# Performance work log

Measured on AMD Instinct MI355X. Metric: run time of the kernel, lower is better.

The kernel has to match this reference:

```python
import jax, jax.numpy as jnp
import numpy as np

N, IN_DIM, OUT_DIM, HEADS = 8192, 256, 128, 2


def setup_inputs() -> dict:
    key = jax.random.key(0)
    k1, k2, k3, k4, k5 = jax.random.split(key, 5)
    features = jax.random.normal(k1, (N, IN_DIM), dtype=jnp.float32)
    adjacency = jax.random.randint(k2, (N, N), 0, 2, dtype=jnp.int32)
    # nn.Linear(input_dim, output_dim*heads, bias=False): weight [out, in]
    W = jax.random.normal(k3, (OUT_DIM * HEADS, IN_DIM), dtype=jnp.float32) * 0.05
    attn_src = jax.random.normal(k4, (HEADS, OUT_DIM), dtype=jnp.float32) * 0.05
    attn_dst = jax.random.normal(k5, (HEADS, OUT_DIM), dtype=jnp.float32) * 0.05
    return {"features": features, "adjacency": adjacency, "W": W,
            "attn_src": attn_src, "attn_dst": attn_dst}


def reference(features, adjacency, W, attn_src, attn_dst):
    n = features.shape[0]
    # transformed: [N, H, F]
    transformed = (features @ W.T).reshape(n, HEADS, OUT_DIM)
    src_scores = jnp.einsum('nhf,hf->nh', transformed, attn_src)  # [N, H]
    dst_scores = jnp.einsum('nhf,hf->nh', transformed, attn_dst)  # [N, H]
    # logits: [N_src, N_dst, H]
    logits = jax.nn.leaky_relu(src_scores[:, None, :] + dst_scores[None, :, :],
                               negative_slope=0.2)
    mask = adjacency > 0  # [N, N]
    logits = jnp.where(mask[:, :, None], logits, -jnp.inf)
    attention = jax.nn.softmax(logits, axis=1)  # softmax over dst dim (dim=1)
    attention = jnp.nan_to_num(attention, nan=0.0, posinf=0.0, neginf=0.0)
    aggregated = jnp.einsum('ijh,jhf->ihf', attention, transformed)  # [N, H, F]
    return aggregated.mean(axis=1)  # [N, F]
```

## Files before the change

kernel.cpp:

```cpp
#include <hip/hip_runtime.h>
#include <stdint.h>
#include <stddef.h>

#define NN 8192
#define KD 256
#define CD 256
#define FD 128
#define BI 32
#define BJ 64
#define JSPLIT 2
#define JCHUNK (NN / JSPLIT)

typedef __attribute__((ext_vector_type(4))) float f32x4;
typedef __attribute__((ext_vector_type(8))) short b16x8;

__device__ __forceinline__ unsigned short f2bf(float x) {
    unsigned int u = __float_as_uint(x);
    u += 0x7fffu + ((u >> 16) & 1u);
    return (unsigned short)(u >> 16);
}

__global__ __launch_bounds__(256) void k_transform(
    const float* __restrict__ feat, const float* __restrict__ W,
    float* __restrict__ T)
{
    __shared__ unsigned short a_lds[64 * 32];
    __shared__ unsigned short b_lds[256 * 32];
    const int t = threadIdx.x;
    const int wave = t >> 6, lane = t & 63;
    const int l15 = lane & 15, quad = lane >> 4;
    const int n0 = blockIdx.x * 64;
    const int ai = t >> 2, ag = t & 3;

    f32x4 acc[4][4] = {};
    for (int kc = 0; kc < 8; ++kc) {
        const int k0 = kc * 32;
        __syncthreads();
        {
            const float* src = feat + (size_t)(n0 + ai) * KD + k0 + ag * 8;
            const float4 v0 = *(const float4*)src;
            const float4 v1 = *(const float4*)(src + 4);
            union { unsigned short us[8]; b16x8 v; } pk;
            pk.us[0] = f2bf(v0.x); pk.us[1] = f2bf(v0.y);
            pk.us[2] = f2bf(v0.z); pk.us[3] = f2bf(v0.w);
            pk.us[4] = f2bf(v1.x); pk.us[5] = f2bf(v1.y);
            pk.us[6] = f2bf(v1.z); pk.us[7] = f2bf(v1.w);
            const int slot = ag ^ ((ai >> 1) & 3);
            *(b16x8*)&a_lds[ai * 32 + slot * 8] = pk.v;
        }
        for (int p = 0; p < 4; ++p) {
            const int G = p * 256 + t;
            const int c = G >> 2, g = G & 3;
            const float* src = W + (size_t)c * KD + k0 + g * 8;
            const float4 v0 = *(const float4*)src;
            const float4 v1 = *(const float4*)(src + 4);
            union { unsigned short us[8]; b16x8 v; } pk;
            pk.us[0] = f2bf(v0.x); pk.us[1] = f2bf(v0.y);
            pk.us[2] = f2bf(v0.z); pk.us[3] = f2bf(v0.w);
            pk.us[4] = f2bf(v1.x); pk.us[5] = f2bf(v1.y);
            pk.us[6] = f2bf(v1.z); pk.us[7] = f2bf(v1.w);
            const int slot = g ^ ((c >> 1) & 3);
            *(b16x8*)&b_lds[c * 32 + slot * 8] = pk.v;
        }
        __syncthreads();
        b16x8 af[4], bfr[4];
        for (int mt = 0; mt < 4; ++mt) {
            const int m = mt * 16 + l15;
            af[mt] = *(const b16x8*)&a_lds[m * 32 + (quad ^ ((m >> 1) & 3)) * 8];
        }
        for (int nt = 0; nt < 4; ++nt) {
            const int c = wave * 64 + nt * 16 + l15;
            bfr[nt] = *(const b16x8*)&b_lds[c * 32 + (quad ^ ((c >> 1) & 3)) * 8];
        }
        for (int mt = 0; mt < 4; ++mt)
            for (int nt = 0; nt < 4; ++nt)
                acc[mt][nt] = __builtin_amdgcn_mfma_f32_16x16x32_bf16(
                    af[mt], bfr[nt], acc[mt][nt], 0, 0, 0);
    }
    for (int mt = 0; mt < 4; ++mt)
        for (int nt = 0; nt < 4; ++nt)
            for (int r = 0; r < 4; ++r) {
                const int n = n0 + mt * 16 + quad * 4 + r;
                const int c = wave * 64 + nt * 16 + l15;
                T[(size_t)n * CD + c] = acc[mt][nt][r];
            }
}

__global__ __launch_bounds__(256) void k_scores(
    const float* __restrict__ T, const float* __restrict__ asrc,
    const float* __restrict__ adst, float* __restrict__ s, float* __restrict__ dsc)
{
    const int wave = threadIdx.x >> 6, lane = threadIdx.x & 63;
    const int n = blockIdx.x * 4 + wave;
    const float* tr = T + (size_t)n * CD;
    const float t0 = tr[lane], t1 = tr[lane + 64], t2 = tr[lane + 128], t3 = tr[lane + 192];
    float s0 = t0 * asrc[lane] + t1 * asrc[lane + 64];
    float s1 = t2 * asrc[128 + lane] + t3 * asrc[192 + lane];
    float d0 = t0 * adst[lane] + t1 * adst[lane + 64];
    float d1 = t2 * adst[128 + lane] + t3 * adst[192 + lane];
    for (int m = 1; m < 64; m <<= 1) {
        s0 += __shfl_xor(s0, m); s1 += __shfl_xor(s1, m);
        d0 += __shfl_xor(d0, m); d1 += __shfl_xor(d1, m);
    }
    if (lane == 0) {
        s[n * 2 + 0] = s0; s[n * 2 + 1] = s1;
        dsc[n * 2 + 0] = d0; dsc[n * 2 + 1] = d1;
    }
}

__global__ __launch_bounds__(256) void k_transpose(
    const float* __restrict__ T, unsigned short* __restrict__ Tt)
{
    __shared__ float tile[64][65];
    const int t = threadIdx.x;
    const int n0 = blockIdx.x * 64, c0 = blockIdx.y * 64;
    for (int p = 0; p < 4; ++p) {
        const int idx = p * 256 + t;
        const int r = idx >> 4, q = idx & 15;
        const float4 v = *(const float4*)(T + (size_t)(n0 + r) * CD + c0 + q * 4);
        tile[r][q * 4 + 0] = v.x; tile[r][q * 4 + 1] = v.y;
        tile[r][q * 4 + 2] = v.z; tile[r][q * 4 + 3] = v.w;
    }
    __syncthreads();
    for (int p = 0; p < 16; ++p) {
        const int idx = p * 256 + t;
        const int c = idx >> 6, n = idx & 63;
        Tt[(size_t)(c0 + c) * NN + n0 + n] = f2bf(tile[n][c]);
    }
}

__global__ __launch_bounds__(256) void k_gat(
    const int* __restrict__ adj, const unsigned short* __restrict__ Tt,
    const float* __restrict__ s, const float* __restrict__ d,
    float* __restrict__ num_part,
    float* __restrict__ den_part)
{
    __shared__ unsigned short tt_lds[CD * BJ];
    __shared__ unsigned short w_lds[2 * BI * BJ];
    __shared__ float d_lds[2][BJ];

    const int t = threadIdx.x;
    const int wave = t >> 6, lane = t & 63;
    const int l15 = lane & 15, quad = lane >> 4;
    const int i0 = blockIdx.x * BI;
    const int chunk = blockIdx.y;
    const int jbase = chunk * JCHUNK;

    const int wi = t >> 3;
    const int j8 = t & 7;
    const int gi = i0 + wi;
    const float s0 = s[gi * 2 + 0];
    const float s1 = s[gi * 2 + 1];

    const int h = wave >> 1;
    const int fh = wave & 1;
    const int cbase = h * 128 + fh * 64;

    f32x4 acc[2][4] = {};
    float den0 = 0.f, den1 = 0.f;

    for (int jt = 0; jt < JCHUNK / BJ; ++jt) {
        const int j0 = jbase + jt * BJ;
        __syncthreads();
        for (int p = 0; p < 8; ++p) {
            const int G = p * 256 + t;
            const int c = G >> 3, g = G & 7;
            const b16x8 v = *(const b16x8*)(Tt + (size_t)c * NN + j0 + g * 8);
            *(b16x8*)&tt_lds[c * BJ + ((g ^ (c & 7)) << 3)] = v;
        }
        if (t < 128) d_lds[t & 1][t >> 1] = d[(j0 + (t >> 1)) * 2 + (t & 1)];
        const int* arow = adj + (size_t)gi * NN + j0 + j8 * 8;
        const int4 a0 = *(const int4*)arow;
        const int4 a1 = *(const int4*)(arow + 4);
        __syncthreads();
        const int am[8] = {a0.x, a0.y, a0.z, a0.w, a1.x, a1.y, a1.z, a1.w};
        union { unsigned short us[8]; b16x8 v; } w0, w1;
        float dp0 = 0.f, dp1 = 0.f;
        for (int e = 0; e < 8; ++e) {
            const float dd0 = d_lds[0][j8 * 8 + e];
            const float dd1 = d_lds[1][j8 * 8 + e];
            float x0 = s0 + dd0;  x0 = x0 > 0.f ? x0 : 0.2f * x0;
            float x1 = s1 + dd1;  x1 = x1 > 0.f ? x1 : 0.2f * x1;
            const float e0 = am[e] != 0 ? __expf(x0) : 0.f;
            const float e1 = am[e] != 0 ? __expf(x1) : 0.f;
            dp0 += e0; dp1 += e1;
            w0.us[e] = f2bf(e0); w1.us[e] = f2bf(e1);
        }
        den0 += dp0; den1 += dp1;
        const int slot = (j8 ^ (wi & 7)) << 3;
        *(b16x8*)&w_lds[(0 * BI + wi) * BJ + slot] = w0.v;
        *(b16x8*)&w_lds[(1 * BI + wi) * BJ + slot] = w1.v;
        __syncthreads();
        for (int ks = 0; ks < 2; ++ks) {
            const int gidx = ks * 4 + quad;
            b16x8 af[2], bfr[4];
            for (int mt = 0; mt < 2; ++mt) {
                const int m = mt * 16 + l15;
                af[mt] = *(const b16x8*)&w_lds[(h * BI + m) * BJ + ((gidx ^ (m & 7)) << 3)];
            }
            for (int nt = 0; nt < 4; ++nt) {
                const int c = cbase + nt * 16 + l15;
                bfr[nt] = *(const b16x8*)&tt_lds[c * BJ + ((gidx ^ (c & 7)) << 3)];
            }
            for (int mt = 0; mt < 2; ++mt)
                for (int nt = 0; nt < 4; ++nt)
                    acc[mt][nt] = __builtin_amdgcn_mfma_f32_16x16x32_bf16(
                        af[mt], bfr[nt], acc[mt][nt], 0, 0, 0);
        }
    }
    den0 += __shfl_xor(den0, 1); den0 += __shfl_xor(den0, 2); den0 += __shfl_xor(den0, 4);
    den1 += __shfl_xor(den1, 1); den1 += __shfl_xor(den1, 2); den1 += __shfl_xor(den1, 4);
    if (j8 == 0) {
        den_part[((size_t)chunk * 2 + 0) * NN + gi] = den0;
        den_part[((size_t)chunk * 2 + 1) * NN + gi] = den1;
    }
    float* np_ = num_part + (size_t)chunk * NN * CD;
    for (int mt = 0; mt < 2; ++mt)
        for (int nt = 0; nt < 4; ++nt)
            for (int r = 0; r < 4; ++r) {
                const int n = i0 + mt * 16 + quad * 4 + r;
                const int c = cbase + nt * 16 + l15;
                np_[(size_t)n * CD + c] = acc[mt][nt][r];
            }
}

__global__ __launch_bounds__(256) void k_combine(
    const float* __restrict__ num_part, const float* __restrict__ den_part,
    float* __restrict__ out)
{
    const int idx = blockIdx.x * 256 + threadIdx.x;
    const int n = idx >> 7, f = idx & 127;
    const size_t row = (size_t)n * CD;
    const float n0 = num_part[row + f] + num_part[(size_t)NN * CD + row + f];
    const float n1 = num_part[row + 128 + f] + num_part[(size_t)NN * CD + row + 128 + f];
    const float d0 = den_part[n] + den_part[2 * NN + n];
    const float d1 = den_part[NN + n] + den_part[3 * NN + n];
    const float r0 = d0 != 0.f ? n0 / d0 : 0.f;
    const float r1 = d1 != 0.f ? n1 / d1 : 0.f;
    out[idx] = 0.5f * (r0 + r1);
}

extern "C" void kernel_launch(void* const* d_in, const int* in_sizes, int n_in,
                              void* d_out, int out_size, void* d_ws, size_t ws_size,
                              hipStream_t stream) {
    const float* feat = (const float*)d_in[0];
    const int*   adj  = (const int*)d_in[1];
    const float* W    = (const float*)d_in[2];
    const float* asrc = (const float*)d_in[3];
    const float* adst = (const float*)d_in[4];
    float* out = (float*)d_out;

    char* ws = (char*)d_ws;
    unsigned short* Tt = (unsigned short*)ws;
    float* T   = (float*)(ws + ((size_t)4 << 20));
    float* s   = (float*)(ws + ((size_t)12 << 20));
    float* dsc = (float*)(ws + ((size_t)12 << 20) + 65536);
    float* den = (float*)(ws + ((size_t)12 << 20) + 131072);
    float* nump= (float*)(ws + ((size_t)12 << 20) + 262144);

    k_transform<<<128, 256, 0, stream>>>(feat, W, T);
    k_scores<<<2048, 256, 0, stream>>>(T, asrc, adst, s, dsc);
    k_transpose<<<dim3(128, 4), 256, 0, stream>>>(T, Tt);
    k_gat<<<dim3(NN / BI, JSPLIT), 256, 0, stream>>>(adj, Tt, s, dsc, nump, den);
    k_combine<<<NN * FD / 256, 256, 0, stream>>>(nump, den, out);
}
```

Measured before the change: 501.8 us.

## Fuse scores and transpose into transform; async LDS loads and wider j-split in GAT

New measurement: 462.6 us. -7.8%, faster.

```diff
diff --git a/kernel.cpp b/kernel.cpp
--- a/kernel.cpp
+++ b/kernel.cpp
@@ -8,8 +8,6 @@
 #define FD 128
 #define BI 32
 #define BJ 64
-#define JSPLIT 2
-#define JCHUNK (NN / JSPLIT)
 
 typedef __attribute__((ext_vector_type(4))) float f32x4;
 typedef __attribute__((ext_vector_type(8))) short b16x8;
@@ -20,12 +18,23 @@
     return (unsigned short)(u >> 16);
 }
 
+__device__ __forceinline__ void async16(const void* g, void* l) {
+    __builtin_amdgcn_global_load_lds(
+        (const __attribute__((address_space(1))) unsigned int*)g,
+        (__attribute__((address_space(3))) unsigned int*)l, 16, 0, 0);
+}
+
 __global__ __launch_bounds__(256) void k_transform(
     const float* __restrict__ feat, const float* __restrict__ W,
-    float* __restrict__ T)
+    const float* __restrict__ asrc, const float* __restrict__ adst,
+    unsigned short* __restrict__ Tt, float* __restrict__ s, float* __restrict__ d)
 {
     __shared__ unsigned short a_lds[64 * 32];
     __shared__ unsigned short b_lds[256 * 32];
+    __shared__ unsigned short tr_lds[256 * 72];
+    __shared__ float sc_lds[4][64];
+    __shared__ float dc_lds[4][64];
+
     const int t = threadIdx.x;
     const int wave = t >> 6, lane = t & 63;
     const int l15 = lane & 15, quad = lane >> 4;
@@ -77,80 +86,70 @@
                 acc[mt][nt] = __builtin_amdgcn_mfma_f32_16x16x32_bf16(
                     af[mt], bfr[nt], acc[mt][nt], 0, 0, 0);
     }
+
+    float aS[4], aD[4];
+    for (int nt = 0; nt < 4; ++nt) {
+        const int c = wave * 64 + nt * 16 + l15;
+        aS[nt] = asrc[c]; aD[nt] = adst[c];
+    }
+    for (int mt = 0; mt < 4; ++mt)
+        for (int r = 0; r < 4; ++r) {
+            float vs = 0.f, vd = 0.f;
+            for (int nt = 0; nt < 4; ++nt) {
+                const float x = acc[mt][nt][r];
+                vs += x * aS[nt]; vd += x * aD[nt];
+            }
+            vs += __shfl_xor(vs, 1); vd += __shfl_xor(vd, 1);
+            vs += __shfl_xor(vs, 2); vd += __shfl_xor(vd, 2);
+            vs += __shfl_xor(vs, 4); vd += __shfl_xor(vd, 4);
+            vs += __shfl_xor(vs, 8); vd += __shfl_xor(vd, 8);
+            if (l15 == 0) {
+                const int nl = mt * 16 + quad * 4 + r;
+                sc_lds[wave][nl] = vs; dc_lds[wave][nl] = vd;
+            }
+        }
     for (int mt = 0; mt < 4; ++mt)
         for (int nt = 0; nt < 4; ++nt)
             for (int r = 0; r < 4; ++r) {
-                const int n = n0 + mt * 16 + quad * 4 + r;
                 const int c = wave * 64 + nt * 16 + l15;
-                T[(size_t)n * CD + c] = acc[mt][nt][r];
-            }
-}
-
-__global__ __launch_bounds__(256) void k_scores(
-    const float* __restrict__ T, const float* __restrict__ asrc,
-    const float* __restrict__ adst, float* __restrict__ s, float* __restrict__ dsc)
-{
-    const int wave = threadIdx.x >> 6, lane = threadIdx.x & 63;
-    const int n = blockIdx.x * 4 + wave;
-    const float* tr = T + (size_t)n * CD;
-    const float t0 = tr[lane], t1 = tr[lane + 64], t2 = tr[lane + 128], t3 = tr[lane + 192];
-    float s0 = t0 * asrc[lane] + t1 * asrc[lane + 64];
-    float s1 = t2 * asrc[128 + lane] + t3 * asrc[192 + lane];
-    float d0 = t0 * adst[lane] + t1 * adst[lane + 64];
-    float d1 = t2 * adst[128 + lane] + t3 * adst[192 + lane];
-    for (int m = 1; m < 64; m <<= 1) {
-        s0 += __shfl_xor(s0, m); s1 += __shfl_xor(s1, m);
-        d0 += __shfl_xor(d0, m); d1 += __shfl_xor(d1, m);
-    }
-    if (lane == 0) {
-        s[n * 2 + 0] = s0; s[n * 2 + 1] = s1;
-        dsc[n * 2 + 0] = d0; dsc[n * 2 + 1] = d1;
-    }
-}
-
-__global__ __launch_bounds__(256) void k_transpose(
-    const float* __restrict__ T, unsigned short* __restrict__ Tt)
-{
-    __shared__ float tile[64][65];
-    const int t = threadIdx.x;
-    const int n0 = blockIdx.x * 64, c0 = blockIdx.y * 64;
-    for (int p = 0; p < 4; ++p) {
+                const int n = mt * 16 + quad * 4 + r;
+                tr_lds[c * 72 + n] = f2bf(acc[mt][nt][r]);
+            }
+    __syncthreads();
+    if (t < 128) {
+        const int n = t >> 1, h = t & 1;
+        s[(size_t)(n0 + n) * 2 + h] = sc_lds[h * 2][n] + sc_lds[h * 2 + 1][n];
+        d[(size_t)(n0 + n) * 2 + h] = dc_lds[h * 2][n] + dc_lds[h * 2 + 1][n];
+    }
+    for (int p = 0; p < 8; ++p) {
         const int idx = p * 256 + t;
-        const int r = idx >> 4, q = idx & 15;
-        const float4 v = *(const float4*)(T + (size_t)(n0 + r) * CD + c0 + q * 4);
-        tile[r][q * 4 + 0] = v.x; tile[r][q * 4 + 1] = v.y;
-        tile[r][q * 4 + 2] = v.z; tile[r][q * 4 + 3] = v.w;
-    }
-    __syncthreads();
-    for (int p = 0; p < 16; ++p) {
-        const int idx = p * 256 + t;
-        const int c = idx >> 6, n = idx & 63;
-        Tt[(size_t)(c0 + c) * NN + n0 + n] = f2bf(tile[n][c]);
-    }
-}
-
-__global__ __launch_bounds__(256) void k_gat(
+        const int c = idx >> 3, g = idx & 7;
+        *(b16x8*)(Tt + (size_t)c * NN + n0 + g * 8) = *(const b16x8*)&tr_lds[c * 72 + g * 8];
+    }
+}
+
+__global__ __launch_bounds__(256, 4) void k_gat(
     const int* __restrict__ adj, const unsigned short* __restrict__ Tt,
     const float* __restrict__ s, const float* __restrict__ d,
     float* __restrict__ num_part,
-    float* __restrict__ den_part)
+    float* __restrict__ den_part,
+    int jchunk)
 {
     __shared__ unsigned short tt_lds[CD * BJ];
     __shared__ unsigned short w_lds[2 * BI * BJ];
-    __shared__ float d_lds[2][BJ];
 
     const int t = threadIdx.x;
     const int wave = t >> 6, lane = t & 63;
     const int l15 = lane & 15, quad = lane >> 4;
     const int i0 = blockIdx.x * BI;
     const int chunk = blockIdx.y;
-    const int jbase = chunk * JCHUNK;
+    const int jbase = chunk * jchunk;
 
     const int wi = t >> 3;
     const int j8 = t & 7;
     const int gi = i0 + wi;
-    const float s0 = s[gi * 2 + 0];
-    const float s1 = s[gi * 2 + 1];
+    const float s0 = s[(size_t)gi * 2 + 0];
+    const float s1 = s[(size_t)gi * 2 + 1];
 
     const int h = wave >> 1;
     const int fh = wave & 1;
@@ -158,29 +157,30 @@
 
     f32x4 acc[2][4] = {};
     float den0 = 0.f, den1 = 0.f;
-
-    for (int jt = 0; jt < JCHUNK / BJ; ++jt) {
+    const int njt = jchunk / BJ;
+
+    for (int jt = 0; jt < njt; ++jt) {
         const int j0 = jbase + jt * BJ;
         __syncthreads();
-        for (int p = 0; p < 8; ++p) {
-            const int G = p * 256 + t;
-            const int c = G >> 3, g = G & 7;
-            const b16x8 v = *(const b16x8*)(Tt + (size_t)c * NN + j0 + g * 8);
-            *(b16x8*)&tt_lds[c * BJ + ((g ^ (c & 7)) << 3)] = v;
-        }
-        if (t < 128) d_lds[t & 1][t >> 1] = d[(j0 + (t >> 1)) * 2 + (t & 1)];
         const int* arow = adj + (size_t)gi * NN + j0 + j8 * 8;
         const int4 a0 = *(const int4*)arow;
         const int4 a1 = *(const int4*)(arow + 4);
-        __syncthreads();
+        const float4* dvp = (const float4*)(d + (size_t)(j0 + j8 * 8) * 2);
+        union { float4 v[4]; float f[16]; } dv;
+        dv.v[0] = dvp[0]; dv.v[1] = dvp[1]; dv.v[2] = dvp[2]; dv.v[3] = dvp[3];
+        for (int p = 0; p < 8; ++p) {
+            const int G = (p * 4 + wave) * 64 + lane;
+            const int c = G >> 3, gt = G & 7;
+            const int g = gt ^ (c & 7);
+            async16(Tt + (size_t)c * NN + j0 + g * 8,
+                    (char*)tt_lds + (size_t)(p * 4 + wave) * 1024);
+        }
         const int am[8] = {a0.x, a0.y, a0.z, a0.w, a1.x, a1.y, a1.z, a1.w};
         union { unsigned short us[8]; b16x8 v; } w0, w1;
         float dp0 = 0.f, dp1 = 0.f;
         for (int e = 0; e < 8; ++e) {
-            const float dd0 = d_lds[0][j8 * 8 + e];
-            const float dd1 = d_lds[1][j8 * 8 + e];
-            float x0 = s0 + dd0;  x0 = x0 > 0.f ? x0 : 0.2f * x0;
-            float x1 = s1 + dd1;  x1 = x1 > 0.f ? x1 : 0.2f * x1;
+            float x0 = s0 + dv.f[e * 2 + 0];  x0 = x0 > 0.f ? x0 : 0.2f * x0;
+            float x1 = s1 + dv.f[e * 2 + 1];  x1 = x1 > 0.f ? x1 : 0.2f * x1;
             const float e0 = am[e] != 0 ? __expf(x0) : 0.f;
             const float e1 = am[e] != 0 ? __expf(x1) : 0.f;
             dp0 += e0; dp1 += e1;
@@ -226,15 +226,19 @@
 
 __global__ __launch_bounds__(256) void k_combine(
     const float* __restrict__ num_part, const float* __restrict__ den_part,
-    float* __restrict__ out)
+    float* __restrict__ out, int jsplit)
 {
     const int idx = blockIdx.x * 256 + threadIdx.x;
     const int n = idx >> 7, f = idx & 127;
     const size_t row = (size_t)n * CD;
-    const float n0 = num_part[row + f] + num_part[(size_t)NN * CD + row + f];
-    const float n1 = num_part[row + 128 + f] + num_part[(size_t)NN * CD + row + 128 + f];
-    const float d0 = den_part[n] + den_part[2 * NN + n];
-    const float d1 = den_part[NN + n] + den_part[3 * NN + n];
+    float n0 = 0.f, n1 = 0.f, d0 = 0.f, d1 = 0.f;
+    for (int c = 0; c < jsplit; ++c) {
+        const size_t base = (size_t)c * NN * CD;
+        n0 += num_part[base + row + f];
+        n1 += num_part[base + row + 128 + f];
+        d0 += den_part[((size_t)c * 2 + 0) * NN + n];
+        d1 += den_part[((size_t)c * 2 + 1) * NN + n];
+    }
     const float r0 = d0 != 0.f ? n0 / d0 : 0.f;
     const float r1 = d1 != 0.f ? n1 / d1 : 0.f;
     out[idx] = 0.5f * (r0 + r1);
@@ -250,17 +254,17 @@
     const float* adst = (const float*)d_in[4];
     float* out = (float*)d_out;
 
+    const int jsplit = (ws_size >= ((size_t)40 << 20)) ? 4 : 2;
+    const int jchunk = NN / jsplit;
+
     char* ws = (char*)d_ws;
     unsigned short* Tt = (unsigned short*)ws;
-    float* T   = (float*)(ws + ((size_t)4 << 20));
-    float* s   = (float*)(ws + ((size_t)12 << 20));
-    float* dsc = (float*)(ws + ((size_t)12 << 20) + 65536);
-    float* den = (float*)(ws + ((size_t)12 << 20) + 131072);
-    float* nump= (float*)(ws + ((size_t)12 << 20) + 262144);
-
-    k_transform<<<128, 256, 0, stream>>>(feat, W, T);
-    k_scores<<<2048, 256, 0, stream>>>(T, asrc, adst, s, dsc);
-    k_transpose<<<dim3(128, 4), 256, 0, stream>>>(T, Tt);
-    k_gat<<<dim3(NN / BI, JSPLIT), 256, 0, stream>>>(adj, Tt, s, dsc, nump, den);
-    k_combine<<<NN * FD / 256, 256, 0, stream>>>(nump, den, out);
-}
+    float* s    = (float*)(ws + ((size_t)4 << 20));
+    float* dsc  = (float*)(ws + ((size_t)4 << 20) + (64 << 10));
+    float* den  = (float*)(ws + ((size_t)4 << 20) + (128 << 10));
+    float* nump = (float*)(ws + ((size_t)8 << 20));
+
+    k_transform<<<128, 256, 0, stream>>>(feat, W, asrc, adst, Tt, s, dsc);
+    k_gat<<<dim3(NN / BI, jsplit), 256, 0, stream>>>(adj, Tt, s, dsc, nump, den, jchunk);
+    k_combine<<<NN * FD / 256, 256, 0, stream>>>(nump, den, out, jsplit);
+}
```
